# Kernel tuning notes

Measured on AMD Instinct MI355X. Metric: run time of the kernel, lower is better.

Reference implementation:

```python
import jax, jax.numpy as jnp
import numpy as np

TEMPERATURE = 0.07
MSE_WEIGHT = 0.5
SUPCON_WEIGHT = 1.0
EPS = 1e-12  # F.normalize default eps

P_POS = 4000
P_NEG = 4000
NVOX = 32768
FEAT = 128


def setup_inputs() -> dict:
    key = jax.random.key(0)
    k1, k2, k3, k4, k5 = jax.random.split(key, 5)
    Zs = jax.random.normal(k1, (1, FEAT, NVOX), dtype=jnp.float32)
    pos_idx = jax.random.randint(k2, (P_POS,), 0, NVOX, dtype=jnp.int32)
    neg_idx = jax.random.randint(k3, (P_NEG,), 0, NVOX, dtype=jnp.int32)
    feature_diff = jax.random.normal(k4, (1, FEAT, 32, 32, 32), dtype=jnp.float32)
    input_diff = jax.random.normal(k5, (1, FEAT, 32, 32, 32), dtype=jnp.float32)
    return {"Zs": Zs, "pos_idx": pos_idx, "neg_idx": neg_idx,
            "feature_diff": feature_diff, "input_diff": input_diff}


def _l2_normalize_rows(x):
    # F.normalize(x, dim=1): x / max(||x||_2, eps)
    n = jnp.sqrt(jnp.sum(x * x, axis=1, keepdims=True))
    return x / jnp.maximum(n, EPS)


def _supcon_loss(Zs, pos_idx, neg_idx):
    feats = Zs[0].T                                   # [Nvox, F]
    pixels = jnp.concatenate([feats[pos_idx], feats[neg_idx]], axis=0)  # [N, F]
    n = pixels.shape[0]
    labels = jnp.concatenate([jnp.ones((P_POS,), jnp.int32),
                              jnp.zeros((P_NEG,), jnp.int32)])
    pixels = _l2_normalize_rows(pixels)
    dot = jnp.matmul(pixels, pixels.T) / TEMPERATURE  # [N, N]
    dot = _l2_normalize_rows(dot)                     # row-normalize the NxN matrix
    expm = jnp.exp(dot)
    class_mask = (labels[:, None] == labels[None, :]) & ~jnp.eye(n, dtype=bool)
    pos_term = expm * class_mask
    pos_term = jnp.where(pos_term == 0, 1.0, pos_term)
    denom = jnp.sum(expm * ~class_mask, axis=1) - jnp.diagonal(expm)  # [N]
    full_term = jnp.log(pos_term) - jnp.log(denom)[None, :]
    return -(1.0 / n) * jnp.sum(full_term)


def reference(Zs, pos_idx, neg_idx, feature_diff, input_diff):
    supcon = _supcon_loss(Zs, pos_idx, neg_idx)
    mse = jnp.mean((feature_diff - input_diff) ** 2)
    return SUPCON_WEIGHT * supcon + MSE_WEIGHT * mse
```

## Files before the change

kernel.cpp:

```cpp
#include <hip/hip_runtime.h>
#include <hip/hip_bf16.h>
#include <math.h>

typedef unsigned short u16;
typedef float  f32x4  __attribute__((ext_vector_type(4)));
typedef __bf16 bf16x8 __attribute__((ext_vector_type(8)));

#define NPOS   4000
#define LDP    136
#define TILE_CH 2176
#define MSE_N  4194304
#define GATHER_B 256
#define MSE_B    512
#define TLD    132

__device__ __forceinline__ void load_lds16(const void* g, void* l) {
  __builtin_amdgcn_global_load_lds(
      (const __attribute__((address_space(1))) unsigned int*)g,
      (__attribute__((address_space(3))) unsigned int*)l, 16, 0, 0);
}

__device__ __forceinline__ float bf2f(u16 h) {
  unsigned u = ((unsigned)h) << 16;
  return __builtin_bit_cast(float, u);
}

struct Args {
  const float* Zs; const int* pos; const int* neg;
  const float4* fd; const float4* idf;
  u16* Pc; u16* Prow; float* G; float* S;
  float* qpos; float* qneg; float* sdpos; float* sdneg;
  float* msepart; float* out;
};

__global__ __launch_bounds__(256) void prep_k(Args a) {
  __shared__ __align__(16) float tile[128 * TLD];
  __shared__ int mlist[1024];
  __shared__ int mcnt;
  int blk = blockIdx.x, tid = threadIdx.x;
  int wave = tid >> 6, lane = tid & 63;
  if (blk < GATHER_B) {
    int v0 = blk << 7;
    if (tid == 0) mcnt = 0;
    __syncthreads();
    {
      int rq = tid >> 5;
      int c4 = (tid & 31) << 2;
      #pragma unroll
      for (int p = 0; p < 16; ++p) {
        int f = p * 8 + rq;
        float4 v = *(const float4*)(a.Zs + ((size_t)f << 15) + v0 + c4);
        *(float4*)&tile[f * TLD + c4] = v;
      }
    }
    for (int k = 0; k < 4000; k += 256) {
      int i = k + tid;
      if (i < 4000) {
        unsigned dp = (unsigned)(a.pos[i] - v0);
        if (dp < 128u) { int m = atomicAdd(&mcnt, 1); mlist[m] = (i << 7) | dp; }
        unsigned dn = (unsigned)(a.neg[i] - v0);
        if (dn < 128u) { int m = atomicAdd(&mcnt, 1); mlist[m] = ((4096 + i) << 7) | dn; }
      }
    }
    __syncthreads();
    int nm = mcnt;
    for (int m = wave; m < nm; m += 4) {
      int e = mlist[m];
      int col = e >> 7, lv = e & 127;
      float x0 = tile[lane * TLD + lv];
      float x1 = tile[(lane + 64) * TLD + lv];
      float s = x0 * x0 + x1 * x1;
      #pragma unroll
      for (int o = 1; o < 64; o <<= 1) s += __shfl_xor(s, o, 64);
      float inv = 1.0f / fmaxf(sqrtf(s), 1e-12f);
      __hip_bfloat16 h0 = __float2bfloat16(x0 * inv);
      __hip_bfloat16 h1 = __float2bfloat16(x1 * inv);
      u16 b0 = *(u16*)&h0, b1 = *(u16*)&h1;
      a.Prow[(size_t)col * LDP + lane]      = b0;
      a.Prow[(size_t)col * LDP + lane + 64] = b1;
      size_t cbase = (size_t)(col >> 7) * (128 * LDP) + (col & 127);
      a.Pc[cbase + (size_t)lane * LDP]        = b0;
      a.Pc[cbase + (size_t)(lane + 64) * LDP] = b1;
    }
  } else if (blk < GATHER_B + MSE_B) {
    int b = blk - GATHER_B;
    float ms = 0.f;
    for (int idx = b * 256 + tid; idx < MSE_N / 4; idx += MSE_B * 256) {
      float4 u = a.fd[idx], w = a.idf[idx];
      float dx = u.x - w.x, dy = u.y - w.y, dz = u.z - w.z, dv = u.w - w.w;
      ms += dx * dx + dy * dy + dz * dz + dv * dv;
    }
    #pragma unroll
    for (int o = 1; o < 64; o <<= 1) ms += __shfl_xor(ms, o, 64);
    __shared__ float red[4];
    if (lane == 0) red[wave] = ms;
    __syncthreads();
    if (tid == 0) a.msepart[b] = red[0] + red[1] + red[2] + red[3];
  } else if (blk < GATHER_B + MSE_B + 2) {
    int ch = (blk == GATHER_B + MSE_B) ? 31 : 63;
    for (int e = tid; e < 128 * 96; e += 256) {
      int f = e / 96, c = 32 + e % 96;
      a.Pc[(size_t)ch * (128 * LDP) + (size_t)f * LDP + c] = 0;
    }
  } else {
    int b = blk - (GATHER_B + MSE_B + 2);
    float4 z = {0.f, 0.f, 0.f, 0.f};
    for (int i = b * 256 + tid; i < 8256; i += 512) ((float4*)a.G)[i] = z;
  }
}

__global__ __launch_bounds__(256) void syrk_k(Args a) {
  __shared__ __align__(16) u16 T0[128 * LDP];
  int blk = blockIdx.x, tid = threadIdx.x;
  int wave = tid >> 6, lane = tid & 63;
  int wm = (wave >> 1) << 6, wn = (wave & 1) << 6;
  int r = lane & 15, q = lane >> 4;
  int sf = tid >> 1, sh = tid & 1;
  float ssum = 0.f;
  f32x4 acc[4][4];
  #pragma unroll
  for (int x = 0; x < 4; ++x)
    #pragma unroll
    for (int y = 0; y < 4; ++y) {
      acc[x][y][0] = 0.f; acc[x][y][1] = 0.f; acc[x][y][2] = 0.f; acc[x][y][3] = 0.f;
    }
  for (int it = 0; it < 4; ++it) {
    const u16* g = a.Pc + (size_t)(blk * 4 + it) * (128 * LDP);
    #pragma unroll
    for (int k = 0; k < 9; ++k) {
      int cc = k * 256 + tid;
      if (cc < TILE_CH) load_lds16(g + cc * 8, &T0[cc * 8]);
    }
    __syncthreads();
    #pragma unroll
    for (int kk = 0; kk < 4; ++kk) {
      int k0 = kk * 32 + q * 8;
      bf16x8 af[4], bfr[4];
      #pragma unroll
      for (int t = 0; t < 4; ++t) {
        af[t]  = *(const bf16x8*)&T0[(wm + t * 16 + r) * LDP + k0];
        bfr[t] = *(const bf16x8*)&T0[(wn + t * 16 + r) * LDP + k0];
      }
      #pragma unroll
      for (int mt = 0; mt < 4; ++mt)
        #pragma unroll
        for (int nt = 0; nt < 4; ++nt)
          acc[mt][nt] = __builtin_amdgcn_mfma_f32_16x16x32_bf16(
              af[mt], bfr[nt], acc[mt][nt], 0, 0, 0);
    }
    {
      const u16* base = &T0[sf * LDP + sh * 64];
      #pragma unroll
      for (int vb = 0; vb < 8; ++vb) {
        bf16x8 v = *(const bf16x8*)&base[vb * 8];
        #pragma unroll
        for (int j = 0; j < 8; ++j) ssum += (float)v[j];
      }
    }
    __syncthreads();
  }
  float* Gf = a.G + (size_t)(blk >> 3) * 16384;
  #pragma unroll
  for (int mt = 0; mt < 4; ++mt)
    #pragma unroll
    for (int nt = 0; nt < 4; ++nt)
      #pragma unroll
      for (int reg = 0; reg < 4; ++reg) {
        int ar = wm + mt * 16 + q * 4 + reg;
        int bc = wn + nt * 16 + r;
        atomicAdd(&Gf[ar * 128 + bc], acc[mt][nt][reg]);
      }
  ssum += __shfl_xor(ssum, 1, 64);
  if (sh == 0) atomicAdd(&a.S[(blk >> 3) * 128 + sf], ssum);
}

__global__ __launch_bounds__(256) void quad_k(Args a) {
  __shared__ __align__(16) u16 T0[128 * LDP];
  __shared__ __align__(16) u16 T1[128 * LDP];
  __shared__ float Sl[256];
  __shared__ float qld[2][128];
  int cb = blockIdx.x & 63, set = blockIdx.x >> 6, tid = threadIdx.x;
  Sl[tid] = a.S[tid];
  const u16* gP = a.Prow + (size_t)cb * (128 * LDP);
  #pragma unroll
  for (int k = 0; k < 9; ++k) {
    int cc = k * 256 + tid;
    if (cc < TILE_CH) load_lds16(gP + cc * 8, &T1[cc * 8]);
  }
  {
    int f = tid >> 1, half = (tid & 1) * 64;
    const float4* gsrc = (const float4*)(a.G + (size_t)set * 16384 + f * 128 + half);
    #pragma unroll
    for (int j16 = 0; j16 < 16; ++j16) {
      float4 v = gsrc[j16];
      __hip_bfloat16 c0 = __float2bfloat16(v.x), c1 = __float2bfloat16(v.y);
      __hip_bfloat16 c2 = __float2bfloat16(v.z), c3 = __float2bfloat16(v.w);
      ushort4 pk = { *(u16*)&c0, *(u16*)&c1, *(u16*)&c2, *(u16*)&c3 };
      *(ushort4*)&T0[f * LDP + half + j16 * 4] = pk;
    }
  }
  __syncthreads();
  int wave = tid >> 6, lane = tid & 63;
  int wm = (wave >> 1) << 6, wn = (wave & 1) << 6;
  int r = lane & 15, q = lane >> 4;
  f32x4 acc[4][4];
  #pragma unroll
  for (int x = 0; x < 4; ++x)
    #pragma unroll
    for (int y = 0; y < 4; ++y) {
      acc[x][y][0] = 0.f; acc[x][y][1] = 0.f; acc[x][y][2] = 0.f; acc[x][y][3] = 0.f;
    }
  #pragma unroll
  for (int kk = 0; kk < 4; ++kk) {
    int k0 = kk * 32 + q * 8;
    bf16x8 af[4], bfr[4];
    #pragma unroll
    for (int t = 0; t < 4; ++t) {
      af[t]  = *(const bf16x8*)&T0[(wm + t * 16 + r) * LDP + k0];
      bfr[t] = *(const bf16x8*)&T1[(wn + t * 16 + r) * LDP + k0];
    }
    #pragma unroll
    for (int mt = 0; mt < 4; ++mt)
      #pragma unroll
      for (int nt = 0; nt < 4; ++nt)
        acc[mt][nt] = __builtin_amdgcn_mfma_f32_16x16x32_bf16(
            af[mt], bfr[nt], acc[mt][nt], 0, 0, 0);
  }
  float qv[4] = {0.f, 0.f, 0.f, 0.f};
  #pragma unroll
  for (int nt = 0; nt < 4; ++nt) {
    int il = wn + nt * 16 + r;
    #pragma unroll
    for (int mt = 0; mt < 4; ++mt) {
      const u16* pp = &T1[il * LDP + wm + mt * 16 + q * 4];
      #pragma unroll
      for (int reg = 0; reg < 4; ++reg)
        qv[nt] += acc[mt][nt][reg] * bf2f(pp[reg]);
    }
  }
  #pragma unroll
  for (int nt = 0; nt < 4; ++nt) {
    qv[nt] += __shfl_xor(qv[nt], 16, 64);
    qv[nt] += __shfl_xor(qv[nt], 32, 64);
  }
  int half = wm >> 6;
  if (q == 0) {
    #pragma unroll
    for (int nt = 0; nt < 4; ++nt) qld[half][wn + nt * 16 + r] = qv[nt];
  }
  __syncthreads();
  float* qarr = set ? a.qneg : a.qpos;
  if (tid < 128) qarr[cb * 128 + tid] = qld[0][tid] + qld[1][tid];
  if (set == 0) {
    int which = tid >> 7, sl = tid & 127;
    const float* Sv = &Sl[which * 128];
    float d = 0.f;
    #pragma unroll
    for (int fb = 0; fb < 16; ++fb) {
      const u16* pv = &T1[sl * LDP + fb * 8];
      #pragma unroll
      for (int j = 0; j < 8; ++j) d += Sv[fb * 8 + j] * bf2f(pv[j]);
    }
    (which ? a.sdneg : a.sdpos)[cb * 128 + sl] = d;
  }
}

__global__ __launch_bounds__(256) void final_k(Args a) {
  int tid = threadIdx.x;
  int wave = tid >> 6, lane = tid & 63;
  float lg = 0.f, sm = 0.f;
  for (int col = tid; col < 8192; col += 256) {
    bool isp = col < NPOS;
    bool isn = (col >= 4096) && (col < 4096 + NPOS);
    if (isp || isn) {
      float qp = a.qpos[col], qn = a.qneg[col];
      float c = 1.0f / sqrtf(qp + qn);
      float qo  = isp ? qn : qp;
      float sdo = isp ? a.sdneg[col] : a.sdpos[col];
      float sds = isp ? a.sdpos[col] : a.sdneg[col];
      float denom = 4000.0f + c * sdo + 0.5f * c * c * qo;
      lg += logf(denom);
      sm += c * (sds - 1.0f);
    }
  }
  float ms = a.msepart[tid] + a.msepart[tid + 256];
  #pragma unroll
  for (int o = 1; o < 64; o <<= 1) {
    lg += __shfl_xor(lg, o, 64);
    sm += __shfl_xor(sm, o, 64);
    ms += __shfl_xor(ms, o, 64);
  }
  __shared__ float redf[12];
  if (lane == 0) { redf[wave] = lg; redf[4 + wave] = sm; redf[8 + wave] = ms; }
  __syncthreads();
  if (tid == 0) {
    float lgs = redf[0] + redf[1] + redf[2] + redf[3];
    float sms = redf[4] + redf[5] + redf[6] + redf[7];
    float mss = redf[8] + redf[9] + redf[10] + redf[11];
    a.out[0] = lgs - sms * (1.0f / 8000.0f) + 0.5f * (mss * (1.0f / (float)MSE_N));
  }
}

extern "C" void kernel_launch(void* const* d_in, const int* in_sizes, int n_in,
                              void* d_out, int out_size, void* d_ws, size_t ws_size,
                              hipStream_t stream) {
  char* ws = (char*)d_ws;
  Args args;
  args.Zs  = (const float*)d_in[0];
  args.pos = (const int*)d_in[1];
  args.neg = (const int*)d_in[2];
  args.fd  = (const float4*)d_in[3];
  args.idf = (const float4*)d_in[4];
  args.out = (float*)d_out;

  args.Pc      = (u16*)(ws + 0);
  args.Prow    = (u16*)(ws + 2228224);
  args.G       = (float*)(ws + 4456448);
  args.S       = (float*)(ws + 4587520);
  args.qpos    = (float*)(ws + 4588544);
  args.qneg    = (float*)(ws + 4621312);
  args.sdpos   = (float*)(ws + 4654080);
  args.sdneg   = (float*)(ws + 4686848);
  args.msepart = (float*)(ws + 4719616);

  prep_k<<<GATHER_B + MSE_B + 4, 256, 0, stream>>>(args);
  syrk_k<<<16, 256, 0, stream>>>(args);
  quad_k<<<128, 256, 0, stream>>>(args);
  final_k<<<1, 256, 0, stream>>>(args);
}
```

Before: 132.6 us.

## Split SYRK across 64 blocks with partial buffers and separate reduction kernel

The Gram/SYRK stage previously ran on 16 blocks, each looping over 4 chunks and atomically adding into a zeroed fp32 G and S. It now launches one block per chunk (64 blocks) that write non-atomic partial G and S tiles. A new reduce kernel sums the 32 partials per set and emits a bf16, padded G that quad_k loads directly via global_load_lds instead of converting fp32 in-kernel. This removes atomics and the zeroing pass and adds parallelism, at the cost of an extra kernel launch and roughly 4 MB of partial-buffer traffic.

```diff
diff --git a/kernel.cpp b/kernel.cpp
--- a/kernel.cpp
+++ b/kernel.cpp
@@ -28,7 +28,7 @@
 struct Args {
   const float* Zs; const int* pos; const int* neg;
   const float4* fd; const float4* idf;
-  u16* Pc; u16* Prow; float* G; float* S;
+  u16* Pc; u16* Prow; float* Gpart; float* Spart; u16* Gb; float* S;
   float* qpos; float* qneg; float* sdpos; float* sdneg;
   float* msepart; float* out;
 };
@@ -96,16 +96,12 @@
     if (lane == 0) red[wave] = ms;
     __syncthreads();
     if (tid == 0) a.msepart[b] = red[0] + red[1] + red[2] + red[3];
-  } else if (blk < GATHER_B + MSE_B + 2) {
+  } else {
     int ch = (blk == GATHER_B + MSE_B) ? 31 : 63;
     for (int e = tid; e < 128 * 96; e += 256) {
       int f = e / 96, c = 32 + e % 96;
       a.Pc[(size_t)ch * (128 * LDP) + (size_t)f * LDP + c] = 0;
     }
-  } else {
-    int b = blk - (GATHER_B + MSE_B + 2);
-    float4 z = {0.f, 0.f, 0.f, 0.f};
-    for (int i = b * 256 + tid; i < 8256; i += 512) ((float4*)a.G)[i] = z;
   }
 }
 
@@ -115,8 +111,6 @@
   int wave = tid >> 6, lane = tid & 63;
   int wm = (wave >> 1) << 6, wn = (wave & 1) << 6;
   int r = lane & 15, q = lane >> 4;
-  int sf = tid >> 1, sh = tid & 1;
-  float ssum = 0.f;
   f32x4 acc[4][4];
   #pragma unroll
   for (int x = 0; x < 4; ++x)
@@ -124,42 +118,43 @@
     for (int y = 0; y < 4; ++y) {
       acc[x][y][0] = 0.f; acc[x][y][1] = 0.f; acc[x][y][2] = 0.f; acc[x][y][3] = 0.f;
     }
-  for (int it = 0; it < 4; ++it) {
-    const u16* g = a.Pc + (size_t)(blk * 4 + it) * (128 * LDP);
-    #pragma unroll
-    for (int k = 0; k < 9; ++k) {
-      int cc = k * 256 + tid;
-      if (cc < TILE_CH) load_lds16(g + cc * 8, &T0[cc * 8]);
-    }
-    __syncthreads();
-    #pragma unroll
-    for (int kk = 0; kk < 4; ++kk) {
-      int k0 = kk * 32 + q * 8;
-      bf16x8 af[4], bfr[4];
-      #pragma unroll
-      for (int t = 0; t < 4; ++t) {
-        af[t]  = *(const bf16x8*)&T0[(wm + t * 16 + r) * LDP + k0];
-        bfr[t] = *(const bf16x8*)&T0[(wn + t * 16 + r) * LDP + k0];
-      }
-      #pragma unroll
-      for (int mt = 0; mt < 4; ++mt)
-        #pragma unroll
-        for (int nt = 0; nt < 4; ++nt)
-          acc[mt][nt] = __builtin_amdgcn_mfma_f32_16x16x32_bf16(
-              af[mt], bfr[nt], acc[mt][nt], 0, 0, 0);
-    }
-    {
-      const u16* base = &T0[sf * LDP + sh * 64];
-      #pragma unroll
-      for (int vb = 0; vb < 8; ++vb) {
-        bf16x8 v = *(const bf16x8*)&base[vb * 8];
-        #pragma unroll
-        for (int j = 0; j < 8; ++j) ssum += (float)v[j];
-      }
-    }
-    __syncthreads();
-  }
-  float* Gf = a.G + (size_t)(blk >> 3) * 16384;
+  const u16* g = a.Pc + (size_t)blk * (128 * LDP);
+  #pragma unroll
+  for (int k = 0; k < 9; ++k) {
+    int cc = k * 256 + tid;
+    if (cc < TILE_CH) load_lds16(g + cc * 8, &T0[cc * 8]);
+  }
+  __syncthreads();
+  #pragma unroll
+  for (int kk = 0; kk < 4; ++kk) {
+    int k0 = kk * 32 + q * 8;
+    bf16x8 af[4], bfr[4];
+    #pragma unroll
+    for (int t = 0; t < 4; ++t) {
+      af[t]  = *(const bf16x8*)&T0[(wm + t * 16 + r) * LDP + k0];
+      bfr[t] = *(const bf16x8*)&T0[(wn + t * 16 + r) * LDP + k0];
+    }
+    #pragma unroll
+    for (int mt = 0; mt < 4; ++mt)
+      #pragma unroll
+      for (int nt = 0; nt < 4; ++nt)
+        acc[mt][nt] = __builtin_amdgcn_mfma_f32_16x16x32_bf16(
+            af[mt], bfr[nt], acc[mt][nt], 0, 0, 0);
+  }
+  {
+    int sf = tid >> 1, sh = tid & 1;
+    float ssum = 0.f;
+    const u16* base = &T0[sf * LDP + sh * 64];
+    #pragma unroll
+    for (int vb = 0; vb < 8; ++vb) {
+      bf16x8 v = *(const bf16x8*)&base[vb * 8];
+      #pragma unroll
+      for (int j = 0; j < 8; ++j) ssum += (float)v[j];
+    }
+    ssum += __shfl_xor(ssum, 1, 64);
+    if (sh == 0) a.Spart[blk * 128 + sf] = ssum;
+  }
+  float* Gp = a.Gpart + (size_t)blk * 16384;
   #pragma unroll
   for (int mt = 0; mt < 4; ++mt)
     #pragma unroll
@@ -168,10 +163,33 @@
       for (int reg = 0; reg < 4; ++reg) {
         int ar = wm + mt * 16 + q * 4 + reg;
         int bc = wn + nt * 16 + r;
-        atomicAdd(&Gf[ar * 128 + bc], acc[mt][nt][reg]);
+        Gp[ar * 128 + bc] = acc[mt][nt][reg];
       }
-  ssum += __shfl_xor(ssum, 1, 64);
-  if (sh == 0) atomicAdd(&a.S[(blk >> 3) * 128 + sf], ssum);
+}
+
+__global__ __launch_bounds__(256) void reduce_k(Args a) {
+  int blk = blockIdx.x, tid = threadIdx.x;
+  if (blk < 64) {
+    int set = blk >> 5, f0 = (blk & 31) * 4;
+    #pragma unroll
+    for (int j = 0; j < 2; ++j) {
+      int o = j * 256 + tid;
+      int row = f0 + (o >> 7), col = o & 127;
+      const float* src = a.Gpart + (size_t)set * 32 * 16384 + row * 128 + col;
+      float s = 0.f;
+      #pragma unroll
+      for (int ch = 0; ch < 32; ++ch) s += src[(size_t)ch * 16384];
+      __hip_bfloat16 h = __float2bfloat16(s);
+      a.Gb[(size_t)set * (128 * LDP) + row * LDP + col] = *(u16*)&h;
+    }
+  } else {
+    int set = tid >> 7, f = tid & 127;
+    const float* sp = a.Spart + (size_t)set * 32 * 128 + f;
+    float s = 0.f;
+    #pragma unroll
+    for (int ch = 0; ch < 32; ++ch) s += sp[ch * 128];
+    a.S[tid] = s;
+  }
 }
 
 __global__ __launch_bounds__(256) void quad_k(Args a) {
@@ -187,17 +205,11 @@
     int cc = k * 256 + tid;
     if (cc < TILE_CH) load_lds16(gP + cc * 8, &T1[cc * 8]);
   }
-  {
-    int f = tid >> 1, half = (tid & 1) * 64;
-    const float4* gsrc = (const float4*)(a.G + (size_t)set * 16384 + f * 128 + half);
-    #pragma unroll
-    for (int j16 = 0; j16 < 16; ++j16) {
-      float4 v = gsrc[j16];
-      __hip_bfloat16 c0 = __float2bfloat16(v.x), c1 = __float2bfloat16(v.y);
-      __hip_bfloat16 c2 = __float2bfloat16(v.z), c3 = __float2bfloat16(v.w);
-      ushort4 pk = { *(u16*)&c0, *(u16*)&c1, *(u16*)&c2, *(u16*)&c3 };
-      *(ushort4*)&T0[f * LDP + half + j16 * 4] = pk;
-    }
+  const u16* gG = a.Gb + (size_t)set * (128 * LDP);
+  #pragma unroll
+  for (int k = 0; k < 9; ++k) {
+    int cc = k * 256 + tid;
+    if (cc < TILE_CH) load_lds16(gG + cc * 8, &T0[cc * 8]);
   }
   __syncthreads();
   int wave = tid >> 6, lane = tid & 63;
@@ -315,16 +327,19 @@
 
   args.Pc      = (u16*)(ws + 0);
   args.Prow    = (u16*)(ws + 2228224);
-  args.G       = (float*)(ws + 4456448);
-  args.S       = (float*)(ws + 4587520);
-  args.qpos    = (float*)(ws + 4588544);
-  args.qneg    = (float*)(ws + 4621312);
-  args.sdpos   = (float*)(ws + 4654080);
-  args.sdneg   = (float*)(ws + 4686848);
-  args.msepart = (float*)(ws + 4719616);
-
-  prep_k<<<GATHER_B + MSE_B + 4, 256, 0, stream>>>(args);
-  syrk_k<<<16, 256, 0, stream>>>(args);
+  args.Gpart   = (float*)(ws + 4456448);
+  args.Spart   = (float*)(ws + 8650752);
+  args.Gb      = (u16*)(ws + 8683520);
+  args.S       = (float*)(ws + 8753152);
+  args.qpos    = (float*)(ws + 8754176);
+  args.qneg    = (float*)(ws + 8786944);
+  args.sdpos   = (float*)(ws + 8819712);
+  args.sdneg   = (float*)(ws + 8852480);
+  args.msepart = (float*)(ws + 8885248);
+
+  prep_k<<<GATHER_B + MSE_B + 2, 256, 0, stream>>>(args);
+  syrk_k<<<64, 256, 0, stream>>>(args);
+  reduce_k<<<65, 256, 0, stream>>>(args);
   quad_k<<<128, 256, 0, stream>>>(args);
   final_k<<<1, 256, 0, stream>>>(args);
 }
```

Result: faster. 128.1 us (median of 2 runs) (-3.4%).

## Split Gram SYRK into per-tile blocks, write bf16 Gram, fold final reduction

Applied to the files above, without the earlier changes.

Replaces the 16-block SYRK that atomically accumulated a float Gram matrix with 128 blocks. Each block computes one 16x16 output tile over 32 column chunks, reduces across waves in LDS, and writes the Gram directly in bf16 in the padded layout. This removes the G zeroing, the float atomics and the float-to-bf16 conversion in quad_k, which can now DMA G straight into LDS. The single-block final kernel is folded into quad_k through a last-block-done atomic counter, saving one launch. Each wave now reads its operands straight from global memory without LDS staging, and the counter adds a fence and an atomic per block.

```diff
diff --git a/kernel.cpp b/kernel.cpp
--- a/kernel.cpp
+++ b/kernel.cpp
@@ -28,9 +28,9 @@
 struct Args {
   const float* Zs; const int* pos; const int* neg;
   const float4* fd; const float4* idf;
-  u16* Pc; u16* Prow; float* G; float* S;
+  u16* Pc; u16* Prow; u16* Gb; float* S;
   float* qpos; float* qneg; float* sdpos; float* sdneg;
-  float* msepart; float* out;
+  float* msepart; unsigned* qcnt; float* out;
 };
 
 __global__ __launch_bounds__(256) void prep_k(Args a) {
@@ -96,82 +96,62 @@
     if (lane == 0) red[wave] = ms;
     __syncthreads();
     if (tid == 0) a.msepart[b] = red[0] + red[1] + red[2] + red[3];
-  } else if (blk < GATHER_B + MSE_B + 2) {
+  } else {
     int ch = (blk == GATHER_B + MSE_B) ? 31 : 63;
+    if (blk == GATHER_B + MSE_B && tid == 0) *a.qcnt = 0u;
     for (int e = tid; e < 128 * 96; e += 256) {
       int f = e / 96, c = 32 + e % 96;
       a.Pc[(size_t)ch * (128 * LDP) + (size_t)f * LDP + c] = 0;
     }
-  } else {
-    int b = blk - (GATHER_B + MSE_B + 2);
-    float4 z = {0.f, 0.f, 0.f, 0.f};
-    for (int i = b * 256 + tid; i < 8256; i += 512) ((float4*)a.G)[i] = z;
-  }
-}
-
-__global__ __launch_bounds__(256) void syrk_k(Args a) {
-  __shared__ __align__(16) u16 T0[128 * LDP];
+  }
+}
+
+__global__ __launch_bounds__(256) void gsyrk_k(Args a) {
+  __shared__ float red[4][256];
+  __shared__ float sred[4][16];
   int blk = blockIdx.x, tid = threadIdx.x;
   int wave = tid >> 6, lane = tid & 63;
-  int wm = (wave >> 1) << 6, wn = (wave & 1) << 6;
+  int set = blk >> 6, t64 = blk & 63;
+  int fi = (t64 >> 3) << 4, fj = (t64 & 7) << 4;
   int r = lane & 15, q = lane >> 4;
-  int sf = tid >> 1, sh = tid & 1;
+  const u16* base = a.Pc + (size_t)set * 32 * (128 * LDP);
+  f32x4 acc = {0.f, 0.f, 0.f, 0.f};
   float ssum = 0.f;
-  f32x4 acc[4][4];
-  #pragma unroll
-  for (int x = 0; x < 4; ++x)
-    #pragma unroll
-    for (int y = 0; y < 4; ++y) {
-      acc[x][y][0] = 0.f; acc[x][y][1] = 0.f; acc[x][y][2] = 0.f; acc[x][y][3] = 0.f;
-    }
-  for (int it = 0; it < 4; ++it) {
-    const u16* g = a.Pc + (size_t)(blk * 4 + it) * (128 * LDP);
-    #pragma unroll
-    for (int k = 0; k < 9; ++k) {
-      int cc = k * 256 + tid;
-      if (cc < TILE_CH) load_lds16(g + cc * 8, &T0[cc * 8]);
-    }
-    __syncthreads();
+  const bool diag = (fi == fj);
+  for (int t = wave; t < 32; t += 4) {
+    const u16* tp = base + (size_t)t * (128 * LDP);
     #pragma unroll
     for (int kk = 0; kk < 4; ++kk) {
       int k0 = kk * 32 + q * 8;
-      bf16x8 af[4], bfr[4];
-      #pragma unroll
-      for (int t = 0; t < 4; ++t) {
-        af[t]  = *(const bf16x8*)&T0[(wm + t * 16 + r) * LDP + k0];
-        bfr[t] = *(const bf16x8*)&T0[(wn + t * 16 + r) * LDP + k0];
+      bf16x8 af  = *(const bf16x8*)&tp[(fi + r) * LDP + k0];
+      bf16x8 bfr = *(const bf16x8*)&tp[(fj + r) * LDP + k0];
+      acc = __builtin_amdgcn_mfma_f32_16x16x32_bf16(af, bfr, acc, 0, 0, 0);
+      if (diag) {
+        #pragma unroll
+        for (int j = 0; j < 8; ++j) ssum += (float)af[j];
       }
-      #pragma unroll
-      for (int mt = 0; mt < 4; ++mt)
-        #pragma unroll
-        for (int nt = 0; nt < 4; ++nt)
-          acc[mt][nt] = __builtin_amdgcn_mfma_f32_16x16x32_bf16(
-              af[mt], bfr[nt], acc[mt][nt], 0, 0, 0);
-    }
-    {
-      const u16* base = &T0[sf * LDP + sh * 64];
-      #pragma unroll
-      for (int vb = 0; vb < 8; ++vb) {
-        bf16x8 v = *(const bf16x8*)&base[vb * 8];
-        #pragma unroll
-        for (int j = 0; j < 8; ++j) ssum += (float)v[j];
-      }
-    }
-    __syncthreads();
-  }
-  float* Gf = a.G + (size_t)(blk >> 3) * 16384;
-  #pragma unroll
-  for (int mt = 0; mt < 4; ++mt)
-    #pragma unroll
-    for (int nt = 0; nt < 4; ++nt)
-      #pragma unroll
-      for (int reg = 0; reg < 4; ++reg) {
-        int ar = wm + mt * 16 + q * 4 + reg;
-        int bc = wn + nt * 16 + r;
-        atomicAdd(&Gf[ar * 128 + bc], acc[mt][nt][reg]);
-      }
-  ssum += __shfl_xor(ssum, 1, 64);
-  if (sh == 0) atomicAdd(&a.S[(blk >> 3) * 128 + sf], ssum);
+    }
+  }
+  #pragma unroll
+  for (int g2 = 0; g2 < 4; ++g2) red[wave][lane * 4 + g2] = acc[g2];
+  if (diag) {
+    ssum += __shfl_xor(ssum, 16, 64);
+    ssum += __shfl_xor(ssum, 32, 64);
+    if (q == 0) sred[wave][r] = ssum;
+  }
+  __syncthreads();
+  if (wave == 0) {
+    #pragma unroll
+    for (int g2 = 0; g2 < 4; ++g2) {
+      float v = red[0][lane * 4 + g2] + red[1][lane * 4 + g2]
+              + red[2][lane * 4 + g2] + red[3][lane * 4 + g2];
+      __hip_bfloat16 h = __float2bfloat16(v);
+      a.Gb[(size_t)set * (128 * LDP) + (size_t)(fi + q * 4 + g2) * LDP + (fj + r)] = *(u16*)&h;
+    }
+    if (diag && lane < 16)
+      a.S[set * 128 + fi + lane] =
+          sred[0][lane] + sred[1][lane] + sred[2][lane] + sred[3][lane];
+  }
 }
 
 __global__ __launch_bounds__(256) void quad_k(Args a) {
@@ -187,17 +167,11 @@
     int cc = k * 256 + tid;
     if (cc < TILE_CH) load_lds16(gP + cc * 8, &T1[cc * 8]);
   }
-  {
-    int f = tid >> 1, half = (tid & 1) * 64;
-    const float4* gsrc = (const float4*)(a.G + (size_t)set * 16384 + f * 128 + half);
-    #pragma unroll
-    for (int j16 = 0; j16 < 16; ++j16) {
-      float4 v = gsrc[j16];
-      __hip_bfloat16 c0 = __float2bfloat16(v.x), c1 = __float2bfloat16(v.y);
-      __hip_bfloat16 c2 = __float2bfloat16(v.z), c3 = __float2bfloat16(v.w);
-      ushort4 pk = { *(u16*)&c0, *(u16*)&c1, *(u16*)&c2, *(u16*)&c3 };
-      *(ushort4*)&T0[f * LDP + half + j16 * 4] = pk;
-    }
+  const u16* gG = a.Gb + (size_t)set * (128 * LDP);
+  #pragma unroll
+  for (int k = 0; k < 9; ++k) {
+    int cc = k * 256 + tid;
+    if (cc < TILE_CH) load_lds16(gG + cc * 8, &T0[cc * 8]);
   }
   __syncthreads();
   int wave = tid >> 6, lane = tid & 63;
@@ -263,11 +237,14 @@
     }
     (which ? a.sdneg : a.sdpos)[cb * 128 + sl] = d;
   }
-}
-
-__global__ __launch_bounds__(256) void final_k(Args a) {
-  int tid = threadIdx.x;
-  int wave = tid >> 6, lane = tid & 63;
+  __threadfence();
+  __syncthreads();
+  __shared__ unsigned lastv;
+  if (tid == 0) lastv = atomicAdd(a.qcnt, 1u);
+  __syncthreads();
+  if (lastv != 127u) return;
+  __threadfence();
+  int wv = tid >> 6, lane2 = tid & 63;
   float lg = 0.f, sm = 0.f;
   for (int col = tid; col < 8192; col += 256) {
     bool isp = col < NPOS;
@@ -291,7 +268,7 @@
     ms += __shfl_xor(ms, o, 64);
   }
   __shared__ float redf[12];
-  if (lane == 0) { redf[wave] = lg; redf[4 + wave] = sm; redf[8 + wave] = ms; }
+  if (lane2 == 0) { redf[wv] = lg; redf[4 + wv] = sm; redf[8 + wv] = ms; }
   __syncthreads();
   if (tid == 0) {
     float lgs = redf[0] + redf[1] + redf[2] + redf[3];
@@ -315,16 +292,16 @@
 
   args.Pc      = (u16*)(ws + 0);
   args.Prow    = (u16*)(ws + 2228224);
-  args.G       = (float*)(ws + 4456448);
-  args.S       = (float*)(ws + 4587520);
-  args.qpos    = (float*)(ws + 4588544);
-  args.qneg    = (float*)(ws + 4621312);
-  args.sdpos   = (float*)(ws + 4654080);
-  args.sdneg   = (float*)(ws + 4686848);
-  args.msepart = (float*)(ws + 4719616);
-
-  prep_k<<<GATHER_B + MSE_B + 4, 256, 0, stream>>>(args);
-  syrk_k<<<16, 256, 0, stream>>>(args);
+  args.Gb      = (u16*)(ws + 4456448);
+  args.S       = (float*)(ws + 4526080);
+  args.qpos    = (float*)(ws + 4527104);
+  args.qneg    = (float*)(ws + 4559872);
+  args.sdpos   = (float*)(ws + 4592640);
+  args.sdneg   = (float*)(ws + 4625408);
+  args.msepart = (float*)(ws + 4658176);
+  args.qcnt    = (unsigned*)(ws + 4660224);
+
+  prep_k<<<GATHER_B + MSE_B + 2, 256, 0, stream>>>(args);
+  gsyrk_k<<<128, 256, 0, stream>>>(args);
   quad_k<<<128, 256, 0, stream>>>(args);
-  final_k<<<1, 256, 0, stream>>>(args);
-}
+}
```

After: 140.5 us. +6.0%, slower.
